# Kernel optimization log

Measured on AMD Instinct MI355X. Metric: run time of the kernel, lower is better.

## Reference

```python
import jax, jax.numpy as jnp
import numpy as np

THRESHOLD = 0.5
T = 16777216  # 2**24 timesteps
PERIOD = 256  # note every 256 frames
NOTE_LEN = 200  # offset 200 frames after onset


def setup_inputs() -> dict:
    key = jax.random.key(0)
    k_u, k_e = jax.random.split(key)
    u = jax.random.normal(k_u, (T, 2), dtype=jnp.float32)
    e = jax.random.normal(k_e, (T, 2), dtype=jnp.float32)
    phase = jnp.arange(T, dtype=jnp.int32) % PERIOD
    onsets = (phase == 0).astype(jnp.int32)
    offsets = (phase == NOTE_LEN).astype(jnp.int32)
    return {"u": u, "e": e, "onsets": onsets, "offsets": offsets}


def reference(u, e, onsets, offsets):
    # Vectorized equivalent of the sequential mask build: a timestep is inside
    # a note iff the number of onsets seen so far (inclusive) exceeds the
    # number of offsets seen so far (inclusive). Per-note mask columns are
    # disjoint, so the stacked (T, n_notes) mask reduces to this 1D active mask
    # for both the thresholded count and the normalizer sum(mask).
    cum_on = jnp.cumsum(onsets)
    cum_off = jnp.cumsum(offsets)
    active = (cum_on > cum_off).astype(u.dtype)  # (T,)
    u_f0 = u[:, 0]  # x[0].split(1, -1) -> first channel is f0
    e_f0 = e[:, 0]
    diff = jnp.abs(active * (e_f0 - u_f0))  # mask*|e-u| since mask in {0,1}
    loss = jnp.sum((diff > THRESHOLD).astype(u.dtype)) / jnp.sum(active)
    return loss
```

## Files before the change

### kernel.cpp

```cpp
#include <hip/hip_runtime.h>
#include <math.h>

typedef unsigned long long u64;

constexpr int T_TOTAL = 16777216;
constexpr int TPB     = 256;
constexpr int SEG     = 2048;
constexpr int NSEG    = T_TOTAL / SEG;
constexpr int NBLK    = NSEG / 4;
constexpr int ITERS   = SEG / 128;
constexpr float THRESHOLD = 0.5f;

__global__ void __launch_bounds__(TPB)
k_segsums(const int2* __restrict__ on2, const int2* __restrict__ off2,
          int* __restrict__ segsums) {
    const int lane = threadIdx.x & 63;
    const int wid  = threadIdx.x >> 6;
    const int seg  = blockIdx.x * 4 + wid;
    const int base = seg * (SEG / 2);
    int s = 0;
    #pragma unroll
    for (int g = 0; g < ITERS / 4; ++g) {
        const int i0 = base + g * 256 + lane;
        int2 a0 = on2[i0];       int2 a1 = on2[i0 + 64];
        int2 a2 = on2[i0 + 128]; int2 a3 = on2[i0 + 192];
        int2 c0 = off2[i0];       int2 c1 = off2[i0 + 64];
        int2 c2 = off2[i0 + 128]; int2 c3 = off2[i0 + 192];
        s += (a0.x + a0.y - c0.x - c0.y) + (a1.x + a1.y - c1.x - c1.y)
           + (a2.x + a2.y - c2.x - c2.y) + (a3.x + a3.y - c3.x - c3.y);
    }
    #pragma unroll
    for (int d = 32; d > 0; d >>= 1) s += __shfl_xor(s, d);
    if (lane == 0) segsums[seg] = s;
}

__global__ void __launch_bounds__(TPB)
k_scan(int* __restrict__ segsums) {
    __shared__ int wsum[4];
    const int lane = threadIdx.x & 63;
    const int wid  = threadIdx.x >> 6;
    int vals[NSEG / TPB];
    const int base = threadIdx.x * (NSEG / TPB);
    int s = 0;
    #pragma unroll
    for (int i = 0; i < NSEG / TPB; i++) { vals[i] = segsums[base + i]; s += vals[i]; }
    int x = s;
    #pragma unroll
    for (int d = 1; d < 64; d <<= 1) {
        int y = __shfl_up(x, d);
        if (lane >= d) x += y;
    }
    if (lane == 63) wsum[wid] = x;
    __syncthreads();
    int wbase = 0;
    #pragma unroll
    for (int w = 0; w < 3; w++) if (w < wid) wbase += wsum[w];
    int ex = wbase + (x - s);
    #pragma unroll
    for (int i = 0; i < NSEG / TPB; i++) { int v = vals[i]; segsums[base + i] = ex; ex += v; }
}

#define PROC(a, c, uv, ev)                                                    \
    {                                                                         \
        u64 be_on  = __ballot((a).x != 0);                                    \
        u64 bo_on  = __ballot((a).y != 0);                                    \
        u64 be_off = __ballot((c).x != 0);                                    \
        u64 bo_off = __ballot((c).y != 0);                                    \
        const int de = __popcll(be_on & le) - __popcll(be_off & le);          \
        const int pe = basep + de + __popcll(bo_on & lt) - __popcll(bo_off & lt); \
        const int po = basep + de + __popcll(bo_on & le) - __popcll(bo_off & le); \
        basep += __popcll(be_on) - __popcll(be_off)                           \
               + __popcll(bo_on) - __popcll(bo_off);                          \
        const int a0 = pe > 0, a1 = po > 0;                                   \
        cact += a0 + a1;                                                      \
        if (a0 && fabsf((ev).x - (uv).x) > THRESHOLD) cover++;                \
        if (a1 && fabsf((ev).z - (uv).z) > THRESHOLD) cover++;                \
    }

__global__ void __launch_bounds__(TPB)
k_count(const int2* __restrict__ on2, const int2* __restrict__ off2,
        const float4* __restrict__ u4, const float4* __restrict__ e4,
        const int* __restrict__ segpre, int2* __restrict__ partials) {
    const int lane = threadIdx.x & 63;
    const int wid  = threadIdx.x >> 6;
    const int seg  = blockIdx.x * 4 + wid;
    const int base = seg * (SEG / 2);
    const u64 le = (~0ull) >> (63 - lane);
    const u64 lt = le >> 1;

    int basep = segpre[seg];
    int cover = 0, cact = 0;

    #pragma unroll
    for (int g = 0; g < ITERS / 4; ++g) {
        const int i0 = base + g * 256 + lane;
        int2   a0 = on2[i0];        int2   a1 = on2[i0 + 64];
        int2   a2 = on2[i0 + 128];  int2   a3 = on2[i0 + 192];
        int2   c0 = off2[i0];       int2   c1 = off2[i0 + 64];
        int2   c2 = off2[i0 + 128]; int2   c3 = off2[i0 + 192];
        float4 u0 = u4[i0];         float4 u1 = u4[i0 + 64];
        float4 u2 = u4[i0 + 128];   float4 u3 = u4[i0 + 192];
        float4 e0 = e4[i0];         float4 e1 = e4[i0 + 64];
        float4 e2 = e4[i0 + 128];   float4 e3 = e4[i0 + 192];
        PROC(a0, c0, u0, e0);
        PROC(a1, c1, u1, e1);
        PROC(a2, c2, u2, e2);
        PROC(a3, c3, u3, e3);
    }

    #pragma unroll
    for (int d = 32; d > 0; d >>= 1) {
        cover += __shfl_xor(cover, d);
        cact  += __shfl_xor(cact, d);
    }
    __shared__ int sc[4], sa[4];
    if (lane == 0) { sc[wid] = cover; sa[wid] = cact; }
    __syncthreads();
    if (threadIdx.x == 0)
        partials[blockIdx.x] = make_int2(sc[0] + sc[1] + sc[2] + sc[3],
                                         sa[0] + sa[1] + sa[2] + sa[3]);
}

__global__ void __launch_bounds__(TPB)
k_final(const int2* __restrict__ partials, float* __restrict__ out) {
    const int lane = threadIdx.x & 63;
    const int wid  = threadIdx.x >> 6;
    int c = 0, a = 0;
    for (int i = threadIdx.x; i < NBLK; i += TPB) {
        int2 p = partials[i];
        c += p.x; a += p.y;
    }
    #pragma unroll
    for (int d = 32; d > 0; d >>= 1) {
        c += __shfl_xor(c, d);
        a += __shfl_xor(a, d);
    }
    __shared__ int sc[4], sa[4];
    if (lane == 0) { sc[wid] = c; sa[wid] = a; }
    __syncthreads();
    if (threadIdx.x == 0) {
        float ctot = (float)(sc[0] + sc[1] + sc[2] + sc[3]);
        float atot = (float)(sa[0] + sa[1] + sa[2] + sa[3]);
        out[0] = ctot / atot;
    }
}

extern "C" void kernel_launch(void* const* d_in, const int* in_sizes, int n_in,
                              void* d_out, int out_size, void* d_ws, size_t ws_size,
                              hipStream_t stream) {
    const float* u   = (const float*)d_in[0];
    const float* e   = (const float*)d_in[1];
    const int*   on  = (const int*)d_in[2];
    const int*   off = (const int*)d_in[3];

    int*  segsums  = (int*)d_ws;
    int2* partials = (int2*)(segsums + NSEG);

    k_segsums<<<NBLK, TPB, 0, stream>>>((const int2*)on, (const int2*)off, segsums);
    k_scan<<<1, TPB, 0, stream>>>(segsums);
    k_count<<<NBLK, TPB, 0, stream>>>((const int2*)on, (const int2*)off,
                                      (const float4*)u, (const float4*)e,
                                      segsums, partials);
    k_final<<<1, TPB, 0, stream>>>(partials, (float*)d_out);
}
```

Baseline: 91.36 us.

## Cache onset/offset ballot masks in the first pass to skip rereading them

The first pass now computes per-wavefront ballot masks of on>off and off>on for even and odd elements, plus running per-iteration prefix bases, and writes them to workspace. The counting pass then reads these compact masks (about 4.5MB) instead of reloading the full onset/offset int arrays (128MB). This cuts the second pass's HBM traffic substantially. It needs a larger workspace, and when the workspace is too small it falls back to the old path.

Result: slower. 96.41 us (+5.5%).

```diff
diff --git a/kernel.cpp b/kernel.cpp
--- a/kernel.cpp
+++ b/kernel.cpp
@@ -11,6 +11,119 @@
 constexpr int ITERS   = SEG / 128;
 constexpr float THRESHOLD = 0.5f;
 
+#define MPROC(a, c)                                                           \
+    {                                                                         \
+        u64 pe_ = __ballot((a).x > (c).x);                                    \
+        u64 ne_ = __ballot((c).x > (a).x);                                    \
+        u64 po_ = __ballot((a).y > (c).y);                                    \
+        u64 no_ = __ballot((c).y > (a).y);                                    \
+        if (lane == 0) ibases[rec] = ssum;                                    \
+        u64 v = pe_;                                                          \
+        v = (lane == 1) ? ne_ : v;                                            \
+        v = (lane == 2) ? po_ : v;                                            \
+        v = (lane == 3) ? no_ : v;                                            \
+        if (lane < 4) ballots[(size_t)rec * 4 + lane] = v;                    \
+        ssum += __popcll(pe_) - __popcll(ne_) + __popcll(po_) - __popcll(no_);\
+        rec++;                                                                \
+    }
+
+__global__ void __launch_bounds__(TPB)
+k_masks(const int2* __restrict__ on2, const int2* __restrict__ off2,
+        u64* __restrict__ ballots, int* __restrict__ ibases,
+        int* __restrict__ segsums) {
+    const int lane = threadIdx.x & 63;
+    const int wid  = threadIdx.x >> 6;
+    const int seg  = blockIdx.x * 4 + wid;
+    const int base = seg * (SEG / 2);
+    int ssum = 0;
+    int rec  = seg * ITERS;
+    #pragma unroll
+    for (int g = 0; g < ITERS / 4; ++g) {
+        const int i0 = base + g * 256 + lane;
+        int2 a0 = on2[i0];        int2 a1 = on2[i0 + 64];
+        int2 a2 = on2[i0 + 128];  int2 a3 = on2[i0 + 192];
+        int2 c0 = off2[i0];       int2 c1 = off2[i0 + 64];
+        int2 c2 = off2[i0 + 128]; int2 c3 = off2[i0 + 192];
+        MPROC(a0, c0);
+        MPROC(a1, c1);
+        MPROC(a2, c2);
+        MPROC(a3, c3);
+    }
+    if (lane == 0) segsums[seg] = ssum;
+}
+
+__global__ void __launch_bounds__(TPB)
+k_scan(int* __restrict__ segsums) {
+    __shared__ int wsum[4];
+    const int lane = threadIdx.x & 63;
+    const int wid  = threadIdx.x >> 6;
+    int vals[NSEG / TPB];
+    const int base = threadIdx.x * (NSEG / TPB);
+    int s = 0;
+    #pragma unroll
+    for (int i = 0; i < NSEG / TPB; i++) { vals[i] = segsums[base + i]; s += vals[i]; }
+    int x = s;
+    #pragma unroll
+    for (int d = 1; d < 64; d <<= 1) {
+        int y = __shfl_up(x, d);
+        if (lane >= d) x += y;
+    }
+    if (lane == 63) wsum[wid] = x;
+    __syncthreads();
+    int wbase = 0;
+    #pragma unroll
+    for (int w = 0; w < 3; w++) if (w < wid) wbase += wsum[w];
+    int ex = wbase + (x - s);
+    #pragma unroll
+    for (int i = 0; i < NSEG / TPB; i++) { int v = vals[i]; segsums[base + i] = ex; ex += v; }
+}
+
+__global__ void __launch_bounds__(TPB)
+k_count2(const float4* __restrict__ u4, const float4* __restrict__ e4,
+         const ulonglong2* __restrict__ bb, const int* __restrict__ ibases,
+         const int* __restrict__ segpre, int2* __restrict__ partials) {
+    const int lane = threadIdx.x & 63;
+    const int wid  = threadIdx.x >> 6;
+    const int seg  = blockIdx.x * 4 + wid;
+    const int base = seg * (SEG / 2);
+    const u64 le = (~0ull) >> (63 - lane);
+    const u64 lt = le >> 1;
+
+    const int sp = segpre[seg];
+    const ulonglong2* mybb = bb + (size_t)seg * ITERS * 2;
+    const int* myib = ibases + seg * ITERS;
+
+    int cover = 0, cact = 0;
+    #pragma unroll 4
+    for (int it = 0; it < ITERS; ++it) {
+        const int idx = base + it * 64 + lane;
+        float4 uv = u4[idx];
+        float4 ev = e4[idx];
+        ulonglong2 w01 = mybb[2 * it];
+        ulonglong2 w23 = mybb[2 * it + 1];
+        const int bp = sp + myib[it];
+        const int de = __popcll(w01.x & le) - __popcll(w01.y & le);
+        const int pe = bp + de + __popcll(w23.x & lt) - __popcll(w23.y & lt);
+        const int po = bp + de + __popcll(w23.x & le) - __popcll(w23.y & le);
+        const int a0 = pe > 0, a1 = po > 0;
+        cact += a0 + a1;
+        if (a0 && fabsf(ev.x - uv.x) > THRESHOLD) cover++;
+        if (a1 && fabsf(ev.z - uv.z) > THRESHOLD) cover++;
+    }
+
+    #pragma unroll
+    for (int d = 32; d > 0; d >>= 1) {
+        cover += __shfl_xor(cover, d);
+        cact  += __shfl_xor(cact, d);
+    }
+    __shared__ int sc[4], sa[4];
+    if (lane == 0) { sc[wid] = cover; sa[wid] = cact; }
+    __syncthreads();
+    if (threadIdx.x == 0)
+        partials[blockIdx.x] = make_int2(sc[0] + sc[1] + sc[2] + sc[3],
+                                         sa[0] + sa[1] + sa[2] + sa[3]);
+}
+
 __global__ void __launch_bounds__(TPB)
 k_segsums(const int2* __restrict__ on2, const int2* __restrict__ off2,
           int* __restrict__ segsums) {
@@ -22,8 +135,8 @@
     #pragma unroll
     for (int g = 0; g < ITERS / 4; ++g) {
         const int i0 = base + g * 256 + lane;
-        int2 a0 = on2[i0];       int2 a1 = on2[i0 + 64];
-        int2 a2 = on2[i0 + 128]; int2 a3 = on2[i0 + 192];
+        int2 a0 = on2[i0];        int2 a1 = on2[i0 + 64];
+        int2 a2 = on2[i0 + 128];  int2 a3 = on2[i0 + 192];
         int2 c0 = off2[i0];       int2 c1 = off2[i0 + 64];
         int2 c2 = off2[i0 + 128]; int2 c3 = off2[i0 + 192];
         s += (a0.x + a0.y - c0.x - c0.y) + (a1.x + a1.y - c1.x - c1.y)
@@ -32,32 +145,6 @@
     #pragma unroll
     for (int d = 32; d > 0; d >>= 1) s += __shfl_xor(s, d);
     if (lane == 0) segsums[seg] = s;
-}
-
-__global__ void __launch_bounds__(TPB)
-k_scan(int* __restrict__ segsums) {
-    __shared__ int wsum[4];
-    const int lane = threadIdx.x & 63;
-    const int wid  = threadIdx.x >> 6;
-    int vals[NSEG / TPB];
-    const int base = threadIdx.x * (NSEG / TPB);
-    int s = 0;
-    #pragma unroll
-    for (int i = 0; i < NSEG / TPB; i++) { vals[i] = segsums[base + i]; s += vals[i]; }
-    int x = s;
-    #pragma unroll
-    for (int d = 1; d < 64; d <<= 1) {
-        int y = __shfl_up(x, d);
-        if (lane >= d) x += y;
-    }
-    if (lane == 63) wsum[wid] = x;
-    __syncthreads();
-    int wbase = 0;
-    #pragma unroll
-    for (int w = 0; w < 3; w++) if (w < wid) wbase += wsum[w];
-    int ex = wbase + (x - s);
-    #pragma unroll
-    for (int i = 0; i < NSEG / TPB; i++) { int v = vals[i]; segsums[base + i] = ex; ex += v; }
 }
 
 #define PROC(a, c, uv, ev)                                                    \
@@ -87,10 +174,8 @@
     const int base = seg * (SEG / 2);
     const u64 le = (~0ull) >> (63 - lane);
     const u64 lt = le >> 1;
-
     int basep = segpre[seg];
     int cover = 0, cact = 0;
-
     #pragma unroll
     for (int g = 0; g < ITERS / 4; ++g) {
         const int i0 = base + g * 256 + lane;
@@ -107,7 +192,6 @@
         PROC(a2, c2, u2, e2);
         PROC(a3, c3, u3, e3);
     }
-
     #pragma unroll
     for (int d = 32; d > 0; d >>= 1) {
         cover += __shfl_xor(cover, d);
@@ -155,11 +239,24 @@
 
     int*  segsums  = (int*)d_ws;
     int2* partials = (int2*)(segsums + NSEG);
-
-    k_segsums<<<NBLK, TPB, 0, stream>>>((const int2*)on, (const int2*)off, segsums);
-    k_scan<<<1, TPB, 0, stream>>>(segsums);
-    k_count<<<NBLK, TPB, 0, stream>>>((const int2*)on, (const int2*)off,
-                                      (const float4*)u, (const float4*)e,
-                                      segsums, partials);
+    int*  ibases   = (int*)((char*)d_ws + 48 * 1024);
+    u64*  ballots  = (u64*)((char*)d_ws + 560 * 1024);
+
+    const size_t need = 560 * 1024 + (size_t)NSEG * ITERS * 4 * sizeof(u64);
+
+    if (ws_size >= need) {
+        k_masks<<<NBLK, TPB, 0, stream>>>((const int2*)on, (const int2*)off,
+                                          ballots, ibases, segsums);
+        k_scan<<<1, TPB, 0, stream>>>(segsums);
+        k_count2<<<NBLK, TPB, 0, stream>>>((const float4*)u, (const float4*)e,
+                                           (const ulonglong2*)ballots, ibases,
+                                           segsums, partials);
+    } else {
+        k_segsums<<<NBLK, TPB, 0, stream>>>((const int2*)on, (const int2*)off, segsums);
+        k_scan<<<1, TPB, 0, stream>>>(segsums);
+        k_count<<<NBLK, TPB, 0, stream>>>((const int2*)on, (const int2*)off,
+                                          (const float4*)u, (const float4*)e,
+                                          segsums, partials);
+    }
     k_final<<<1, TPB, 0, stream>>>(partials, (float*)d_out);
 }
```
